# Performance work log

Hardware: AMD Instinct MI355X
Metric: run time of the kernel (lower is better)

The kernel has to match this reference:

```python
import jax, jax.numpy as jnp
import numpy as np

K = 60
BATCH, NCLS, H, W = 8, 2, 512, 512


def _neighbors(x):
    # x: [B,H,W] int32 in {0,1}. Returns P2..P9 clockwise starting north.
    p = jnp.pad(x, ((0, 0), (1, 1), (1, 1)))
    P2 = p[:, :-2, 1:-1]   # N
    P3 = p[:, :-2, 2:]     # NE
    P4 = p[:, 1:-1, 2:]    # E
    P5 = p[:, 2:, 2:]      # SE
    P6 = p[:, 2:, 1:-1]    # S
    P7 = p[:, 2:, :-2]     # SW
    P8 = p[:, 1:-1, :-2]   # W
    P9 = p[:, :-2, :-2]    # NW
    return P2, P3, P4, P5, P6, P7, P8, P9


def _substep(x, first):
    # One Zhang-Suen thinning sub-iteration (the algorithm used by
    # skimage.morphology.skeletonize for 2D images).
    P2, P3, P4, P5, P6, P7, P8, P9 = _neighbors(x)
    seq = (P2, P3, P4, P5, P6, P7, P8, P9, P2)
    # A = number of 0->1 transitions in circular neighbor sequence
    A = sum(((seq[i] == 0) & (seq[i + 1] == 1)).astype(jnp.int32) for i in range(8))
    Bn = P2 + P3 + P4 + P5 + P6 + P7 + P8 + P9
    if first:
        c3 = P2 * P4 * P6
        c4 = P4 * P6 * P8
    else:
        c3 = P2 * P4 * P8
        c4 = P2 * P6 * P8
    delete = (x == 1) & (Bn >= 2) & (Bn <= 6) & (A == 1) & (c3 == 0) & (c4 == 0)
    return x * (1 - delete.astype(x.dtype))


def _skeletonize(img):
    # img: [B,H,W] int32 binary. Iterate thinning until fixed point.
    def body(state):
        x, _ = state
        x2 = _substep(_substep(x, True), False)
        return x2, jnp.any(x2 != x)

    def cond(state):
        return state[1]

    out, _ = jax.lax.while_loop(cond, body, (img, jnp.array(True)))
    return out


def _conv(x, kernel, pad):
    # x: [B,1,H,W], kernel: [1,1,k,k], 'same' padding pad
    return jax.lax.conv_general_dilated(x, kernel, (1, 1), [(pad, pad), (pad, pad)])


def setup_inputs() -> dict:
    key = jax.random.key(0)
    k1, k2 = jax.random.split(key)
    pred = jax.random.normal(k1, (BATCH, NCLS, H, W), dtype=jnp.float32)
    target = jax.random.randint(k2, (BATCH, H, W), 0, NCLS, dtype=jnp.int32)
    return {"pred": pred, "target": target}


def reference(pred, target):
    # Per-pixel cross entropy, reduction='none'
    logp = jax.nn.log_softmax(pred, axis=1)
    L = -jnp.take_along_axis(logp, target[:, None].astype(jnp.int32), axis=1)[:, 0]  # [B,H,W]

    # Skeletonize the hard prediction (nonzero = foreground)
    A = jnp.argmax(pred, axis=1)
    skel = _skeletonize((A != 0).astype(jnp.int32))  # [B,H,W]
    Bm = skel[:, None].astype(pred.dtype)            # [B,1,H,W]

    # 3x3 neighbor count (center zeroed); endpoints C where product == 1
    k3 = jnp.ones((1, 1, 3, 3), pred.dtype).at[0, 0, 1, 1].set(0.0)
    C = Bm * _conv(Bm, k3, 1)
    C = (C == 1.0).astype(pred.dtype)

    # 9x9 endpoint density, scaled by K; zeros -> weight 1
    k9 = jnp.ones((1, 1, 9, 9), pred.dtype)
    N = _conv(C, k9, 4) * K
    Wmap = N + (N == 0.0).astype(pred.dtype)  # [B,1,H,W]

    return jnp.mean(Wmap[:, 0] * L)
```

## Files before the change

kernel.cpp:

```cpp
#include <hip/hip_runtime.h>

#define BATCH   8
#define HH      512
#define WW      512
#define IMGPIX  (HH * WW)
#define NPIX    (BATCH * IMGPIX)
#define NWORDS  (NPIX / 64)
#define KFAC    60.0f
#define WPR     8
#define FPSCALE 262144.0

#define BPI     8
#define GZ      8
#define OWN     64
#define ROWS    (OWN + 2 * GZ)
#define STHREADS (ROWS * WPR)
#define LROW    9
#define MAXC    64
#define NBARCHG (BATCH + BATCH * MAXC)

typedef unsigned long long u64;
typedef unsigned int u32;

__global__ void prep_kernel(const float* __restrict__ pred, const int* __restrict__ target,
                            float* __restrict__ L, u64* __restrict__ xp,
                            u64* __restrict__ acc64, u32* __restrict__ ticket,
                            u32* __restrict__ barchg) {
    int i = blockIdx.x * blockDim.x + threadIdx.x;
    if (i == 0) { acc64[0] = 0ULL; ticket[0] = 0u; }
    if (i < NBARCHG) barchg[i] = 0u;
    if (i >= NPIX) return;
    int b = i >> 18;
    int hw = i & (IMGPIX - 1);
    float p0 = pred[((size_t)(2 * b) << 18) + hw];
    float p1 = pred[((size_t)(2 * b + 1) << 18) + hw];
    float m = fmaxf(p0, p1);
    float lse = m + logf(expf(p0 - m) + expf(p1 - m));
    int t = target[i];
    L[i] = lse - (t ? p1 : p0);
    u64 word = __ballot(p1 > p0);
    if ((threadIdx.x & 63) == 0) xp[i >> 6] = word;
}

#define FA(a,b,c,s,cy) { u64 _x = (a)^(b); (s) = _x^(c); (cy) = ((a)&(b)) | ((c)&_x); }
#define HA(a,b,s,cy)   { (s) = (a)^(b); (cy) = (a)&(b); }

__device__ __forceinline__ u64 zs_word(int first,
    u64 Up, u64 Uc, u64 Un, u64 Mp, u64 Mc, u64 Mn, u64 Dp, u64 Dc, u64 Dn,
    u64* delp)
{
    if (Mc == 0ULL) { *delp = 0ULL; return 0ULL; }
    u64 P2 = Uc, P6 = Dc;
    u64 P3 = (Uc >> 1) | (Un << 63);
    u64 P4 = (Mc >> 1) | (Mn << 63);
    u64 P5 = (Dc >> 1) | (Dn << 63);
    u64 P9 = (Uc << 1) | (Up >> 63);
    u64 P8 = (Mc << 1) | (Mp >> 63);
    u64 P7 = (Dc << 1) | (Dp >> 63);

    u64 sa,ca, sb,cb, sc,cc, b0,cd, sd,ce, b1,cf, b2,b3;
    FA(P2,P3,P4, sa,ca);
    FA(P5,P6,P7, sb,cb);
    FA(P8,P9,sa, sc,cc);
    HA(sb,sc,    b0,cd);
    FA(ca,cb,cc, sd,ce);
    HA(sd,cd,    b1,cf);
    HA(ce,cf,    b2,b3);
    u64 ge2 = b1 | b2 | b3;
    u64 le6 = ~(b3 | (b0 & b1 & b2));

    u64 e, seen, two = 0;
    seen = (~P2) & P3;
    e = (~P3) & P4; two |= seen & e; seen |= e;
    e = (~P4) & P5; two |= seen & e; seen |= e;
    e = (~P5) & P6; two |= seen & e; seen |= e;
    e = (~P6) & P7; two |= seen & e; seen |= e;
    e = (~P7) & P8; two |= seen & e; seen |= e;
    e = (~P8) & P9; two |= seen & e; seen |= e;
    e = (~P9) & P2; two |= seen & e; seen |= e;
    u64 A1 = seen & ~two;

    u64 c34;
    if (first) { u64 t = P4 & P6; c34 = t & (P2 | P8); }
    else       { u64 t = P2 & P8; c34 = t & (P4 | P6); }

    u64 del = Mc & ge2 & le6 & A1 & ~c34;
    *delp = del;
    return Mc ^ del;
}

__global__ __launch_bounds__(STHREADS)
void skel_kernel(const u64* __restrict__ xp, u64* __restrict__ xs,
                 u64* __restrict__ eg, u32* __restrict__ bar, u32* __restrict__ chg)
{
    __shared__ u64 lds[2][ROWS * LROW];
    __shared__ u32 sh_ch;
    const int blk  = blockIdx.x;
    const int img  = blk / BPI;
    const int part = blk - img * BPI;
    const int t    = threadIdx.x;
    const int rL   = t >> 3;
    const int wc   = t & 7;
    const int gr0  = part * OWN - GZ;
    const u64* src = xp + ((size_t)img << 12);

    {
        int gr = gr0 + rL;
        lds[0][rL * LROW + wc] = ((unsigned)gr < (unsigned)HH) ? src[gr * WPR + wc] : 0ULL;
        lds[1][rL * LROW + wc] = 0ULL;
    }
    __syncthreads();

    for (int chunk = 0; chunk < MAXC; ++chunk) {
        u32 mych = 0;
        #pragma unroll
        for (int s = 0; s < GZ; ++s) {
            const u64* B = lds[s & 1];
            int base = rL * LROW + wc;
            u64 Mc = B[base];
            u64 Mp = wc       ? B[base - 1] : 0ULL;
            u64 Mn = (wc < 7) ? B[base + 1] : 0ULL;
            u64 Uc = 0, Up = 0, Un = 0, Dc = 0, Dp = 0, Dn = 0;
            if (rL > 0) {
                Uc = B[base - LROW];
                Up = wc       ? B[base - LROW - 1] : 0ULL;
                Un = (wc < 7) ? B[base - LROW + 1] : 0ULL;
            }
            if (rL < ROWS - 1) {
                Dc = B[base + LROW];
                Dp = wc       ? B[base + LROW - 1] : 0ULL;
                Dn = (wc < 7) ? B[base + LROW + 1] : 0ULL;
            }
            u64 del;
            u64 nw = zs_word((s & 1) == 0, Up, Uc, Un, Mp, Mc, Mn, Dp, Dc, Dn, &del);
            lds[(s & 1) ^ 1][base] = nw;
            if (del && rL >= GZ && rL < GZ + OWN) mych = 1;
            __syncthreads();
        }
        u32 blockch = __syncthreads_or(mych);

        u64* xsp = xs + (size_t)(chunk & 1) * NWORDS + ((size_t)img << 12);
        if (t < 2 * GZ * WPR) {
            int k = t >> 3, bwc = t & 7;
            int brL = (k < GZ) ? (GZ + k) : (OWN - GZ + k);
            int gr = gr0 + brL;
            xsp[gr * WPR + bwc] = lds[0][brL * LROW + bwc];
        }
        __syncthreads();
        if (t == 0) {
            if (blockch) atomicOr(&chg[img * MAXC + chunk], 1u);
            __threadfence();
            atomicAdd(&bar[img], 1u);
            u32 tgt = (u32)(BPI * (chunk + 1));
            while (__hip_atomic_load(&bar[img], __ATOMIC_ACQUIRE, __HIP_MEMORY_SCOPE_AGENT) < tgt)
                __builtin_amdgcn_s_sleep(8);
            sh_ch = chg[img * MAXC + chunk];
        }
        __syncthreads();
        u32 anych = sh_ch;
        if (t < 2 * GZ * WPR) {
            int k = t >> 3, bwc = t & 7;
            int grL = (k < GZ) ? k : (OWN + k);
            int gr = gr0 + grL;
            if ((unsigned)gr < (unsigned)HH)
                lds[0][grL * LROW + bwc] = xsp[gr * WPR + bwc];
        }
        __syncthreads();
        if (!anych) break;
    }

    if (rL >= GZ && rL < GZ + OWN) {
        const u64* B = lds[0];
        int base = rL * LROW + wc;
        u64 Mc = B[base];
        u64 Mp = wc       ? B[base - 1] : 0ULL;
        u64 Mn = (wc < 7) ? B[base + 1] : 0ULL;
        u64 Uc = B[base - LROW];
        u64 Up = wc       ? B[base - LROW - 1] : 0ULL;
        u64 Un = (wc < 7) ? B[base - LROW + 1] : 0ULL;
        u64 Dc = B[base + LROW];
        u64 Dp = wc       ? B[base + LROW - 1] : 0ULL;
        u64 Dn = (wc < 7) ? B[base + LROW + 1] : 0ULL;
        u64 P2 = Uc, P6 = Dc;
        u64 P3 = (Uc >> 1) | (Un << 63);
        u64 P4 = (Mc >> 1) | (Mn << 63);
        u64 P5 = (Dc >> 1) | (Dn << 63);
        u64 P9 = (Uc << 1) | (Up >> 63);
        u64 P8 = (Mc << 1) | (Mp >> 63);
        u64 P7 = (Dc << 1) | (Dp >> 63);
        u64 e, seen, two = 0;
        seen = P2;
        e = P3; two |= seen & e; seen |= e;
        e = P4; two |= seen & e; seen |= e;
        e = P5; two |= seen & e; seen |= e;
        e = P6; two |= seen & e; seen |= e;
        e = P7; two |= seen & e; seen |= e;
        e = P8; two |= seen & e; seen |= e;
        e = P9; two |= seen & e; seen |= e;
        eg[((size_t)img << 12) + (size_t)(gr0 + rL) * WPR + wc] = Mc & seen & ~two;
    }
}

struct Planes { u64 p0, p1, p2, p3; };

__device__ __forceinline__ Planes vcount9(const u64 r[9]) {
    u64 s0,c0, s1,c1, s2,c2, p0,t0, t1,t2, p1,t3, p2,p3;
    FA(r[0],r[1],r[2], s0,c0);
    FA(r[3],r[4],r[5], s1,c1);
    FA(r[6],r[7],r[8], s2,c2);
    FA(s0,s1,s2, p0,t0);
    FA(c0,c1,c2, t1,t2);
    HA(t0,t1,    p1,t3);
    HA(t2,t3,    p2,p3);
    Planes P; P.p0 = p0; P.p1 = p1; P.p2 = p2; P.p3 = p3; return P;
}

__device__ __forceinline__ u64 spread8(u64 bb) {
    u64 s = (bb * 0x0101010101010101ULL) & 0x8040201008040201ULL;
    return ((s + 0x7f7f7f7f7f7f7f7fULL) >> 7) & 0x0101010101010101ULL;
}

__device__ __forceinline__ u64 vbytes(const Planes& P, int g) {
    int s = 8 * g;
    return  spread8((P.p0 >> s) & 0xFFULL)
         + (spread8((P.p1 >> s) & 0xFFULL) << 1)
         + (spread8((P.p2 >> s) & 0xFFULL) << 2)
         + (spread8((P.p3 >> s) & 0xFFULL) << 3);
}

__global__ __launch_bounds__(256)
void final_kernel(const float* __restrict__ L, const u64* __restrict__ eg,
                  u64* __restrict__ acc64, u32* __restrict__ ticket,
                  float* __restrict__ out) {
    __shared__ float sm[256];
    int wi = blockIdx.x * blockDim.x + threadIdx.x;
    int b  = wi >> 12;
    int h  = (wi >> 3) & (HH - 1);
    int wc = wi & 7;
    const u64* img = eg + ((size_t)b << 12);

    u64 rows[3][9];
    #pragma unroll
    for (int dh = -4; dh <= 4; ++dh) {
        int hh = h + dh;
        bool okh = (unsigned)hh < (unsigned)HH;
        const u64* rp = img + hh * WPR;
        rows[0][dh + 4] = (okh && wc > 0) ? rp[wc - 1] : 0ULL;
        rows[1][dh + 4] = okh             ? rp[wc]     : 0ULL;
        rows[2][dh + 4] = (okh && wc < 7) ? rp[wc + 1] : 0ULL;
    }
    Planes Pm = vcount9(rows[0]);
    Planes Pc = vcount9(rows[1]);
    Planes Pp = vcount9(rows[2]);

    u64 v[10];
    v[0] = vbytes(Pm, 7);
    #pragma unroll
    for (int g = 0; g < 8; ++g) v[g + 1] = vbytes(Pc, g);
    v[9] = vbytes(Pp, 0);

    const float4* Lr = (const float4*)(L + ((size_t)wi << 6));
    float acc = 0.0f;
    #pragma unroll
    for (int g = 0; g < 8; ++g) {
        u64 a = v[g + 1], lo = v[g], hi = v[g + 2];
        u64 n = a;
        #pragma unroll
        for (int d = 1; d <= 4; ++d) {
            n += (a >> (8 * d)) | (hi << (64 - 8 * d));
            n += (a << (8 * d)) | (lo >> (64 - 8 * d));
        }
        float4 f0 = Lr[2 * g], f1 = Lr[2 * g + 1];
        #pragma unroll
        for (int j = 0; j < 8; ++j) {
            int cnt = (int)((n >> (8 * j)) & 0xFFULL);
            float wgt = cnt ? (float)(60 * cnt) : 1.0f;
            float lv = (j < 4) ? ((j == 0) ? f0.x : (j == 1) ? f0.y : (j == 2) ? f0.z : f0.w)
                               : ((j == 4) ? f1.x : (j == 5) ? f1.y : (j == 6) ? f1.z : f1.w);
            acc += wgt * lv;
        }
    }

    sm[threadIdx.x] = acc;
    __syncthreads();
    for (int s = 128; s > 0; s >>= 1) {
        if (threadIdx.x < s) sm[threadIdx.x] += sm[threadIdx.x + s];
        __syncthreads();
    }
    if (threadIdx.x == 0) {
        u64 vfx = (u64)(long long)llrintf(sm[0] * (float)FPSCALE);
        atomicAdd(acc64, vfx);
        __threadfence();
        u32 t = atomicAdd(ticket, 1u);
        if (t == (u32)(gridDim.x - 1)) {
            __threadfence();
            u64 total = __hip_atomic_load(acc64, __ATOMIC_RELAXED, __HIP_MEMORY_SCOPE_AGENT);
            out[0] = (float)((double)(long long)total / (FPSCALE * (double)NPIX));
        }
    }
}

extern "C" void kernel_launch(void* const* d_in, const int* in_sizes, int n_in,
                              void* d_out, int out_size, void* d_ws, size_t ws_size,
                              hipStream_t stream) {
    const float* pred = (const float*)d_in[0];
    const int* target = (const int*)d_in[1];
    float* out = (float*)d_out;
    char* ws = (char*)d_ws;

    float* L    = (float*)(ws);
    u64* xp     = (u64*)(ws + 8388608);
    u64* eg     = (u64*)(ws + 8650752);
    u64* xs     = (u64*)(ws + 8912896);
    u64* acc64  = (u64*)(ws + 9437184);
    u32* ticket = (u32*)(ws + 9437192);
    u32* bar    = (u32*)(ws + 9437196);
    u32* chg    = (u32*)(ws + 9437228);

    prep_kernel<<<dim3(NPIX / 256), dim3(256), 0, stream>>>(pred, target, L, xp, acc64, ticket, bar);

    {
        void* args[] = { (void*)&xp, (void*)&xs, (void*)&eg, (void*)&bar, (void*)&chg };
        hipLaunchCooperativeKernel((void*)skel_kernel, dim3(BATCH * BPI), dim3(STHREADS),
                                   args, 0, stream);
    }

    final_kernel<<<dim3(NWORDS / 256), dim3(256), 0, stream>>>(L, eg, acc64, ticket, out);
}
```

Measured before the change: 70.14 us.

## Fuse endpoint-weighted loss into skeleton kernel and split images into more blocks

The separate final kernel is removed. Each cooperative skeleton block now computes endpoint bits for its tile plus a 4-row halo in shared memory, then does the 9x9 count, the weighted cross-entropy sum and the atomic final reduction itself. Blocks per image go from 8 to 32, each owning 16 rows. Every block writes all its owned rows to the exchange buffer and reloads only its halo rows. The prep kernel also handles four ballot words per thread. This saves a kernel launch and the global endpoint round trip, and spreads the iteration over more CUs. In exchange, the halo share rises, so more redundant per-substep work is done relative to owned rows, and more blocks take part in each per-image barrier.

```diff
diff --git a/kernel.cpp b/kernel.cpp
--- a/kernel.cpp
+++ b/kernel.cpp
@@ -6,17 +6,17 @@
 #define IMGPIX  (HH * WW)
 #define NPIX    (BATCH * IMGPIX)
 #define NWORDS  (NPIX / 64)
-#define KFAC    60.0f
 #define WPR     8
 #define FPSCALE 262144.0
 
-#define BPI     8
+#define BPI     32
 #define GZ      8
-#define OWN     64
+#define OWN     16
 #define ROWS    (OWN + 2 * GZ)
 #define STHREADS (ROWS * WPR)
 #define LROW    9
 #define MAXC    64
+#define NBLK    (BATCH * BPI)
 #define NBARCHG (BATCH + BATCH * MAXC)
 
 typedef unsigned long long u64;
@@ -26,20 +26,25 @@
                             float* __restrict__ L, u64* __restrict__ xp,
                             u64* __restrict__ acc64, u32* __restrict__ ticket,
                             u32* __restrict__ barchg) {
-    int i = blockIdx.x * blockDim.x + threadIdx.x;
-    if (i == 0) { acc64[0] = 0ULL; ticket[0] = 0u; }
-    if (i < NBARCHG) barchg[i] = 0u;
-    if (i >= NPIX) return;
-    int b = i >> 18;
-    int hw = i & (IMGPIX - 1);
-    float p0 = pred[((size_t)(2 * b) << 18) + hw];
-    float p1 = pred[((size_t)(2 * b + 1) << 18) + hw];
-    float m = fmaxf(p0, p1);
-    float lse = m + logf(expf(p0 - m) + expf(p1 - m));
-    int t = target[i];
-    L[i] = lse - (t ? p1 : p0);
-    u64 word = __ballot(p1 > p0);
-    if ((threadIdx.x & 63) == 0) xp[i >> 6] = word;
+    int j = blockIdx.x * blockDim.x + threadIdx.x;
+    if (j == 0) { acc64[0] = 0ULL; ticket[0] = 0u; }
+    if (j < NBARCHG) barchg[j] = 0u;
+    int lane = j & 63;
+    int pixbase = (j >> 6) << 8;
+    #pragma unroll
+    for (int k = 0; k < 4; ++k) {
+        int i = pixbase + (k << 6) + lane;
+        int b = i >> 18;
+        int hw = i & (IMGPIX - 1);
+        float p0 = pred[((size_t)(2 * b) << 18) + hw];
+        float p1 = pred[((size_t)(2 * b + 1) << 18) + hw];
+        float m = fmaxf(p0, p1);
+        float lse = m + logf(expf(p0 - m) + expf(p1 - m));
+        int t = target[i];
+        L[i] = lse - (t ? p1 : p0);
+        u64 word = __ballot(p1 > p0);
+        if (lane == 0) xp[(pixbase >> 6) + k] = word;
+    }
 }
 
 #define FA(a,b,c,s,cy) { u64 _x = (a)^(b); (s) = _x^(c); (cy) = ((a)&(b)) | ((c)&_x); }
@@ -89,25 +94,57 @@
     return Mc ^ del;
 }
 
+struct Planes { u64 p0, p1, p2, p3; };
+
+__device__ __forceinline__ Planes vcount9(const u64 r[9]) {
+    u64 s0,c0, s1,c1, s2,c2, p0,t0, t1,t2, p1,t3, p2,p3;
+    FA(r[0],r[1],r[2], s0,c0);
+    FA(r[3],r[4],r[5], s1,c1);
+    FA(r[6],r[7],r[8], s2,c2);
+    FA(s0,s1,s2, p0,t0);
+    FA(c0,c1,c2, t1,t2);
+    HA(t0,t1,    p1,t3);
+    HA(t2,t3,    p2,p3);
+    Planes P; P.p0 = p0; P.p1 = p1; P.p2 = p2; P.p3 = p3; return P;
+}
+
+__device__ __forceinline__ u64 spread8(u64 bb) {
+    u64 s = (bb * 0x0101010101010101ULL) & 0x8040201008040201ULL;
+    return ((s + 0x7f7f7f7f7f7f7f7fULL) >> 7) & 0x0101010101010101ULL;
+}
+
+__device__ __forceinline__ u64 vbytes(const Planes& P, int g) {
+    int s = 8 * g;
+    return  spread8((P.p0 >> s) & 0xFFULL)
+         + (spread8((P.p1 >> s) & 0xFFULL) << 1)
+         + (spread8((P.p2 >> s) & 0xFFULL) << 2)
+         + (spread8((P.p3 >> s) & 0xFFULL) << 3);
+}
+
 __global__ __launch_bounds__(STHREADS)
 void skel_kernel(const u64* __restrict__ xp, u64* __restrict__ xs,
-                 u64* __restrict__ eg, u32* __restrict__ bar, u32* __restrict__ chg)
+                 const float* __restrict__ L,
+                 u64* __restrict__ acc64, u32* __restrict__ ticket,
+                 u32* __restrict__ bar, u32* __restrict__ chg,
+                 float* __restrict__ out)
 {
     __shared__ u64 lds[2][ROWS * LROW];
+    __shared__ float sm[STHREADS];
     __shared__ u32 sh_ch;
     const int blk  = blockIdx.x;
-    const int img  = blk / BPI;
-    const int part = blk - img * BPI;
+    const int img  = blk >> 5;
+    const int part = blk & (BPI - 1);
     const int t    = threadIdx.x;
     const int rL   = t >> 3;
     const int wc   = t & 7;
     const int gr0  = part * OWN - GZ;
+    const int base = rL * LROW + wc;
+    const bool owned = (rL >= GZ) && (rL < GZ + OWN);
     const u64* src = xp + ((size_t)img << 12);
 
     {
         int gr = gr0 + rL;
-        lds[0][rL * LROW + wc] = ((unsigned)gr < (unsigned)HH) ? src[gr * WPR + wc] : 0ULL;
-        lds[1][rL * LROW + wc] = 0ULL;
+        lds[0][base] = ((unsigned)gr < (unsigned)HH) ? src[gr * WPR + wc] : 0ULL;
     }
     __syncthreads();
 
@@ -116,7 +153,6 @@
         #pragma unroll
         for (int s = 0; s < GZ; ++s) {
             const u64* B = lds[s & 1];
-            int base = rL * LROW + wc;
             u64 Mc = B[base];
             u64 Mp = wc       ? B[base - 1] : 0ULL;
             u64 Mn = (wc < 7) ? B[base + 1] : 0ULL;
@@ -134,18 +170,13 @@
             u64 del;
             u64 nw = zs_word((s & 1) == 0, Up, Uc, Un, Mp, Mc, Mn, Dp, Dc, Dn, &del);
             lds[(s & 1) ^ 1][base] = nw;
-            if (del && rL >= GZ && rL < GZ + OWN) mych = 1;
+            if (del && owned) mych = 1;
             __syncthreads();
         }
         u32 blockch = __syncthreads_or(mych);
 
         u64* xsp = xs + (size_t)(chunk & 1) * NWORDS + ((size_t)img << 12);
-        if (t < 2 * GZ * WPR) {
-            int k = t >> 3, bwc = t & 7;
-            int brL = (k < GZ) ? (GZ + k) : (OWN - GZ + k);
-            int gr = gr0 + brL;
-            xsp[gr * WPR + bwc] = lds[0][brL * LROW + bwc];
-        }
+        if (owned) xsp[(gr0 + rL) * WPR + wc] = lds[0][base];
         __syncthreads();
         if (t == 0) {
             if (blockch) atomicOr(&chg[img * MAXC + chunk], 1u);
@@ -158,20 +189,18 @@
         }
         __syncthreads();
         u32 anych = sh_ch;
-        if (t < 2 * GZ * WPR) {
-            int k = t >> 3, bwc = t & 7;
-            int grL = (k < GZ) ? k : (OWN + k);
-            int gr = gr0 + grL;
+        if (!owned) {
+            int gr = gr0 + rL;
             if ((unsigned)gr < (unsigned)HH)
-                lds[0][grL * LROW + bwc] = xsp[gr * WPR + bwc];
+                lds[0][base] = xsp[gr * WPR + wc];
         }
         __syncthreads();
         if (!anych) break;
     }
 
-    if (rL >= GZ && rL < GZ + OWN) {
+    u64* Ebuf = lds[1];
+    if (rL >= 4 && rL < 28) {
         const u64* B = lds[0];
-        int base = rL * LROW + wc;
         u64 Mc = B[base];
         u64 Mp = wc       ? B[base - 1] : 0ULL;
         u64 Mn = (wc < 7) ? B[base + 1] : 0ULL;
@@ -197,102 +226,65 @@
         e = P7; two |= seen & e; seen |= e;
         e = P8; two |= seen & e; seen |= e;
         e = P9; two |= seen & e; seen |= e;
-        eg[((size_t)img << 12) + (size_t)(gr0 + rL) * WPR + wc] = Mc & seen & ~two;
-    }
-}
-
-struct Planes { u64 p0, p1, p2, p3; };
-
-__device__ __forceinline__ Planes vcount9(const u64 r[9]) {
-    u64 s0,c0, s1,c1, s2,c2, p0,t0, t1,t2, p1,t3, p2,p3;
-    FA(r[0],r[1],r[2], s0,c0);
-    FA(r[3],r[4],r[5], s1,c1);
-    FA(r[6],r[7],r[8], s2,c2);
-    FA(s0,s1,s2, p0,t0);
-    FA(c0,c1,c2, t1,t2);
-    HA(t0,t1,    p1,t3);
-    HA(t2,t3,    p2,p3);
-    Planes P; P.p0 = p0; P.p1 = p1; P.p2 = p2; P.p3 = p3; return P;
-}
-
-__device__ __forceinline__ u64 spread8(u64 bb) {
-    u64 s = (bb * 0x0101010101010101ULL) & 0x8040201008040201ULL;
-    return ((s + 0x7f7f7f7f7f7f7f7fULL) >> 7) & 0x0101010101010101ULL;
-}
-
-__device__ __forceinline__ u64 vbytes(const Planes& P, int g) {
-    int s = 8 * g;
-    return  spread8((P.p0 >> s) & 0xFFULL)
-         + (spread8((P.p1 >> s) & 0xFFULL) << 1)
-         + (spread8((P.p2 >> s) & 0xFFULL) << 2)
-         + (spread8((P.p3 >> s) & 0xFFULL) << 3);
-}
-
-__global__ __launch_bounds__(256)
-void final_kernel(const float* __restrict__ L, const u64* __restrict__ eg,
-                  u64* __restrict__ acc64, u32* __restrict__ ticket,
-                  float* __restrict__ out) {
-    __shared__ float sm[256];
-    int wi = blockIdx.x * blockDim.x + threadIdx.x;
-    int b  = wi >> 12;
-    int h  = (wi >> 3) & (HH - 1);
-    int wc = wi & 7;
-    const u64* img = eg + ((size_t)b << 12);
-
-    u64 rows[3][9];
-    #pragma unroll
-    for (int dh = -4; dh <= 4; ++dh) {
-        int hh = h + dh;
-        bool okh = (unsigned)hh < (unsigned)HH;
-        const u64* rp = img + hh * WPR;
-        rows[0][dh + 4] = (okh && wc > 0) ? rp[wc - 1] : 0ULL;
-        rows[1][dh + 4] = okh             ? rp[wc]     : 0ULL;
-        rows[2][dh + 4] = (okh && wc < 7) ? rp[wc + 1] : 0ULL;
-    }
-    Planes Pm = vcount9(rows[0]);
-    Planes Pc = vcount9(rows[1]);
-    Planes Pp = vcount9(rows[2]);
-
-    u64 v[10];
-    v[0] = vbytes(Pm, 7);
-    #pragma unroll
-    for (int g = 0; g < 8; ++g) v[g + 1] = vbytes(Pc, g);
-    v[9] = vbytes(Pp, 0);
-
-    const float4* Lr = (const float4*)(L + ((size_t)wi << 6));
+        Ebuf[base] = Mc & seen & ~two;
+    }
+    __syncthreads();
+
     float acc = 0.0f;
-    #pragma unroll
-    for (int g = 0; g < 8; ++g) {
-        u64 a = v[g + 1], lo = v[g], hi = v[g + 2];
-        u64 n = a;
+    if (owned) {
+        u64 rows0[9], rows1[9], rows2[9];
         #pragma unroll
-        for (int d = 1; d <= 4; ++d) {
-            n += (a >> (8 * d)) | (hi << (64 - 8 * d));
-            n += (a << (8 * d)) | (lo >> (64 - 8 * d));
-        }
-        float4 f0 = Lr[2 * g], f1 = Lr[2 * g + 1];
+        for (int dh = -4; dh <= 4; ++dh) {
+            int rr = (rL + dh) * LROW;
+            rows0[dh + 4] = wc       ? Ebuf[rr + wc - 1] : 0ULL;
+            rows1[dh + 4] =            Ebuf[rr + wc];
+            rows2[dh + 4] = (wc < 7) ? Ebuf[rr + wc + 1] : 0ULL;
+        }
+        Planes Pm = vcount9(rows0);
+        Planes Pc = vcount9(rows1);
+        Planes Pp = vcount9(rows2);
+
+        u64 v[10];
+        v[0] = vbytes(Pm, 7);
         #pragma unroll
-        for (int j = 0; j < 8; ++j) {
-            int cnt = (int)((n >> (8 * j)) & 0xFFULL);
-            float wgt = cnt ? (float)(60 * cnt) : 1.0f;
-            float lv = (j < 4) ? ((j == 0) ? f0.x : (j == 1) ? f0.y : (j == 2) ? f0.z : f0.w)
-                               : ((j == 4) ? f1.x : (j == 5) ? f1.y : (j == 6) ? f1.z : f1.w);
-            acc += wgt * lv;
-        }
-    }
-
-    sm[threadIdx.x] = acc;
+        for (int g = 0; g < 8; ++g) v[g + 1] = vbytes(Pc, g);
+        v[9] = vbytes(Pp, 0);
+
+        const float4* Lr = (const float4*)(L + ((size_t)img << 18)
+                                             + (size_t)(gr0 + rL) * WW + (wc << 6));
+        #pragma unroll
+        for (int g = 0; g < 8; ++g) {
+            u64 a = v[g + 1], lo = v[g], hi = v[g + 2];
+            u64 n = a;
+            #pragma unroll
+            for (int d = 1; d <= 4; ++d) {
+                n += (a >> (8 * d)) | (hi << (64 - 8 * d));
+                n += (a << (8 * d)) | (lo >> (64 - 8 * d));
+            }
+            float4 f0 = Lr[2 * g], f1 = Lr[2 * g + 1];
+            #pragma unroll
+            for (int jj = 0; jj < 8; ++jj) {
+                int cnt = (int)((n >> (8 * jj)) & 0xFFULL);
+                float wgt = cnt ? (float)(60 * cnt) : 1.0f;
+                float lv = (jj < 4) ? ((jj == 0) ? f0.x : (jj == 1) ? f0.y : (jj == 2) ? f0.z : f0.w)
+                                    : ((jj == 4) ? f1.x : (jj == 5) ? f1.y : (jj == 6) ? f1.z : f1.w);
+                acc += wgt * lv;
+            }
+        }
+    }
+
+    sm[t] = acc;
     __syncthreads();
-    for (int s = 128; s > 0; s >>= 1) {
-        if (threadIdx.x < s) sm[threadIdx.x] += sm[threadIdx.x + s];
+    for (int s = STHREADS / 2; s > 0; s >>= 1) {
+        if (t < s) sm[t] += sm[t + s];
         __syncthreads();
     }
-    if (threadIdx.x == 0) {
+    if (t == 0) {
         u64 vfx = (u64)(long long)llrintf(sm[0] * (float)FPSCALE);
         atomicAdd(acc64, vfx);
         __threadfence();
-        u32 t = atomicAdd(ticket, 1u);
-        if (t == (u32)(gridDim.x - 1)) {
+        u32 tk = atomicAdd(ticket, 1u);
+        if (tk == (u32)(NBLK - 1)) {
             __threadfence();
             u64 total = __hip_atomic_load(acc64, __ATOMIC_RELAXED, __HIP_MEMORY_SCOPE_AGENT);
             out[0] = (float)((double)(long long)total / (FPSCALE * (double)NPIX));
@@ -310,20 +302,19 @@
 
     float* L    = (float*)(ws);
     u64* xp     = (u64*)(ws + 8388608);
-    u64* eg     = (u64*)(ws + 8650752);
-    u64* xs     = (u64*)(ws + 8912896);
-    u64* acc64  = (u64*)(ws + 9437184);
-    u32* ticket = (u32*)(ws + 9437192);
-    u32* bar    = (u32*)(ws + 9437196);
-    u32* chg    = (u32*)(ws + 9437228);
-
-    prep_kernel<<<dim3(NPIX / 256), dim3(256), 0, stream>>>(pred, target, L, xp, acc64, ticket, bar);
+    u64* xs     = (u64*)(ws + 8650752);
+    u64* acc64  = (u64*)(ws + 9175040);
+    u32* ticket = (u32*)(ws + 9175048);
+    u32* bar    = (u32*)(ws + 9175052);
+    u32* chg    = (u32*)(ws + 9175084);
+
+    prep_kernel<<<dim3(NPIX / 4 / 256), dim3(256), 0, stream>>>(pred, target, L, xp,
+                                                                acc64, ticket, bar);
 
     {
-        void* args[] = { (void*)&xp, (void*)&xs, (void*)&eg, (void*)&bar, (void*)&chg };
-        hipLaunchCooperativeKernel((void*)skel_kernel, dim3(BATCH * BPI), dim3(STHREADS),
+        void* args[] = { (void*)&xp, (void*)&xs, (void*)&L, (void*)&acc64,
+                         (void*)&ticket, (void*)&bar, (void*)&chg, (void*)&out };
+        hipLaunchCooperativeKernel((void*)skel_kernel, dim3(NBLK), dim3(STHREADS),
                                    args, 0, stream);
     }
-
-    final_kernel<<<dim3(NWORDS / 256), dim3(256), 0, stream>>>(L, eg, acc64, ticket, out);
-}
+}
```

Measured after the change: 75.81 us. 8.1% more time.
